# Kernel tuning notes

Hardware: AMD Instinct MI355X
Metric: run time of the kernel (lower is better)

The kernel has to match this reference:

```python
import jax, jax.numpy as jnp
import numpy as np

B, S, D, DV = 1, 4096, 1024, 1024  # S == 4*D required by the data-dependent scale broadcast


def setup_inputs() -> dict:
    key = jax.random.key(0)
    kq, kk, kv, ks, kp = jax.random.split(key, 5)
    return {
        "q": jax.random.normal(kq, (B, S, D), dtype=jnp.float32),
        "k": jax.random.normal(kk, (B, S, D), dtype=jnp.float32),
        "v": jax.random.normal(kv, (B, S, DV), dtype=jnp.float32),
        "scale_factor": jax.random.normal(ks, (1,), dtype=jnp.float32),  # overwritten in forward
        "dropout_p": jax.random.uniform(kp, (1,), dtype=jnp.float32),   # overwritten in forward
    }


def reference(q, k, v, scale_factor, dropout_p):
    b, s, d = q.shape
    step = s // 4
    # data-dependent per-column scale: 4 strided rows of q flattened -> (B, 4*D) == (B, S)
    scale = q[:, ::step].reshape(b, -1)            # (B, S)
    qk = jnp.einsum('bsd,btd->bst', q, k)           # (B, S, S)
    scaled_qk = qk * scale[:, None, :]              # torch broadcast (B,S)->(1,1,S) since B==1
    softmax_qk = jax.nn.softmax(scaled_qk, axis=-1)
    # dropout with tensor p is ill-defined in torch; identity (eval semantics)
    return jnp.einsum('bst,btv->bsv', softmax_qk, v)
```

## Files before the change

kernel.cpp:

```cpp
#include <hip/hip_runtime.h>
#include <hip/hip_bf16.h>

typedef __bf16 bf16x8 __attribute__((ext_vector_type(8)));
typedef __bf16 bf16x4 __attribute__((ext_vector_type(4)));
typedef float f32x4 __attribute__((ext_vector_type(4)));

#define S_LEN 4096
#define DDIM  1024

#define MFMA __builtin_amdgcn_mfma_f32_16x16x32_bf16

#define BAR() do { asm volatile("" ::: "memory"); __builtin_amdgcn_s_barrier(); asm volatile("" ::: "memory"); } while (0)
#define VM6() asm volatile("s_waitcnt vmcnt(6)" ::: "memory")
#define VM0() asm volatile("s_waitcnt vmcnt(0)" ::: "memory")

__device__ __forceinline__ void gl_lds16(const __bf16* g, __bf16* l)
{
    __builtin_amdgcn_global_load_lds(
        (const __attribute__((address_space(1))) void*)g,
        (__attribute__((address_space(3))) void*)l, 16, 0, 0);
}

__global__ void prep_hilo(const float* __restrict__ q, const float* __restrict__ kk,
                          __bf16* __restrict__ qh, __bf16* __restrict__ ql,
                          __bf16* __restrict__ kh, __bf16* __restrict__ kl)
{
    const int n8 = (S_LEN * DDIM) / 8;
    for (int i = blockIdx.x * blockDim.x + threadIdx.x; i < n8; i += gridDim.x * blockDim.x) {
        float4 a = *(const float4*)(q + (size_t)i * 8);
        float4 b = *(const float4*)(q + (size_t)i * 8 + 4);
        float va[8] = {a.x, a.y, a.z, a.w, b.x, b.y, b.z, b.w};
        bf16x8 h, l;
#pragma unroll
        for (int j = 0; j < 8; ++j) {
            __bf16 hh = (__bf16)va[j];
            h[j] = hh;
            l[j] = (__bf16)(va[j] - (float)hh);
        }
        *(bf16x8*)(qh + (size_t)i * 8) = h;
        *(bf16x8*)(ql + (size_t)i * 8) = l;

        a = *(const float4*)(kk + (size_t)i * 8);
        b = *(const float4*)(kk + (size_t)i * 8 + 4);
        float vb[8] = {a.x, a.y, a.z, a.w, b.x, b.y, b.z, b.w};
#pragma unroll
        for (int j = 0; j < 8; ++j) {
            __bf16 hh = (__bf16)vb[j];
            h[j] = hh;
            l[j] = (__bf16)(vb[j] - (float)hh);
        }
        *(bf16x8*)(kh + (size_t)i * 8) = h;
        *(bf16x8*)(kl + (size_t)i * 8) = l;
    }
}

__global__ void prep_vt(const float* __restrict__ v, __bf16* __restrict__ vt)
{
    __shared__ float tile[32][33];
    const int t0 = blockIdx.x * 32;
    const int d0 = blockIdx.y * 32;
    const int tx = threadIdx.x & 31;
    const int ty = threadIdx.x >> 5;
#pragma unroll
    for (int i = 0; i < 32; i += 8)
        tile[ty + i][tx] = v[(size_t)(t0 + ty + i) * DDIM + d0 + tx];
    __syncthreads();
#pragma unroll
    for (int i = 0; i < 32; i += 8)
        vt[(size_t)(d0 + ty + i) * S_LEN + t0 + tx] = (__bf16)tile[tx][ty + i];
}

__global__ void prep_scale(const float* __restrict__ q, float* __restrict__ scale)
{
    const int j = blockIdx.x * blockDim.x + threadIdx.x;
    if (j < S_LEN) scale[j] = q[((size_t)(j >> 10) << 20) + (j & 1023)];
}

__device__ __forceinline__ const __bf16* selA(const __bf16* qh, const __bf16* ql, int ps)
{ return ps == 1 ? ql : qh; }
__device__ __forceinline__ const __bf16* selB(const __bf16* kh, const __bf16* kl, int ps)
{ return ps == 2 ? kl : kh; }

template<int BUF, int RG>
__device__ __forceinline__ void stageG1(__bf16 (&lds)[2][4][8192], const __bf16* pl,
                                        int base, int koff, int w, int lane)
{
#pragma unroll
    for (int j = 0; j < 2; ++j) {
        const int ubase = (2 * w + j) * 64;
        const int u = ubase + lane;
        const int r = u >> 3, cu = u & 7;
        int grow;
        if (RG < 2) grow = base + ((r >> 6) << 7) + ((RG & 1) << 6) + (r & 63);
        else        grow = base + ((r >> 5) << 6) + ((RG & 1) << 5) + (r & 31);
        const __bf16* src = pl + (size_t)grow * DDIM + koff + ((cu ^ (r & 7)) << 3);
        gl_lds16(src, &lds[BUF][RG][0] + ubase * 8);
    }
}

template<int BUF, int MH>
__device__ __forceinline__ void rdA(bf16x8 (&a)[4][2], const __bf16 (&lds)[2][4][8192],
                                    int wr, int arow, int aoct)
{
#pragma unroll
    for (int mi = 0; mi < 4; ++mi)
#pragma unroll
        for (int ks = 0; ks < 2; ++ks) {
            const int lr = wr * 64 + mi * 16 + arow;
            const int cc = ks * 4 + aoct;
            a[mi][ks] = *(const bf16x8*)((const char*)&lds[BUF][MH][0]
                            + lr * 128 + ((cc ^ (lr & 7)) << 4));
        }
}

template<int BUF, int NH>
__device__ __forceinline__ void rdB(bf16x8 (&b)[2][2], const __bf16 (&lds)[2][4][8192],
                                    int wc, int arow, int aoct)
{
#pragma unroll
    for (int ni = 0; ni < 2; ++ni)
#pragma unroll
        for (int ks = 0; ks < 2; ++ks) {
            const int lr = wc * 32 + ni * 16 + arow;
            const int cc = ks * 4 + aoct;
            b[ni][ks] = *(const bf16x8*)((const char*)&lds[BUF][2 + NH][0]
                            + lr * 128 + ((cc ^ (lr & 7)) << 4));
        }
}

#define QMFMA(MH, NH, bb) \
    _Pragma("unroll") for (int ks = 0; ks < 2; ++ks) \
    _Pragma("unroll") for (int mi = 0; mi < 4; ++mi) \
    _Pragma("unroll") for (int ni = 0; ni < 2; ++ni) \
        acc[(MH)*4 + mi][(NH)*2 + ni] = MFMA(a[mi][ks], bb[ni][ks], acc[(MH)*4 + mi][(NH)*2 + ni], 0, 0, 0);

__global__ __launch_bounds__(512, 2) void gemm_qk(
    const __bf16* __restrict__ qh, const __bf16* __restrict__ ql,
    const __bf16* __restrict__ kh, const __bf16* __restrict__ kl,
    const float* __restrict__ scale, float* __restrict__ Sout)
{
    __shared__ __align__(16) __bf16 lds[2][4][8192];

    const int tid = threadIdx.x;
    const int w = tid >> 6, lane = tid & 63;
    const int arow = lane & 15, aoct = lane >> 4;
    const int wr = w >> 2, wc = w & 3;
    const int nb = (blockIdx.x & 7) * 32 + (blockIdx.x >> 3);
    const int m0 = (nb & 15) * 256, n0 = (nb >> 4) * 256;

    f32x4 acc[8][4];
#pragma unroll
    for (int i = 0; i < 8; ++i)
#pragma unroll
        for (int j = 0; j < 4; ++j) acc[i][j] = (f32x4){0.f, 0.f, 0.f, 0.f};

    stageG1<0, 0>(lds, selA(qh, ql, 0), m0, 0, w, lane);
    stageG1<0, 1>(lds, selA(qh, ql, 0), m0, 0, w, lane);
    stageG1<0, 2>(lds, selB(kh, kl, 0), n0, 0, w, lane);
    stageG1<0, 3>(lds, selB(kh, kl, 0), n0, 0, w, lane);
    stageG1<1, 0>(lds, selA(qh, ql, 0), m0, 64, w, lane);
    stageG1<1, 2>(lds, selB(kh, kl, 0), n0, 64, w, lane);
    stageG1<1, 3>(lds, selB(kh, kl, 0), n0, 64, w, lane);
    VM6(); BAR();

    for (int it = 0; it < 24; ++it) {
        const int t0 = 2 * it, t1 = 2 * it + 1;
        const bool last = (it == 23);
        const int ps1 = t1 >> 4, ko1 = (t1 & 15) << 6;
        const int ps2 = (t0 + 2) >> 4, ko2 = ((t0 + 2) & 15) << 6;
        const int ps3 = (t1 + 2) >> 4, ko3 = ((t1 + 2) & 15) << 6;
        bf16x8 a[4][2], b0[2][2], b1[2][2];

        rdA<0, 0>(a, lds, wr, arow, aoct);
        rdB<0, 0>(b0, lds, wc, arow, aoct);
        stageG1<1, 1>(lds, selA(qh, ql, ps1), m0, ko1, w, lane);
        BAR();
        __builtin_amdgcn_s_setprio(1); QMFMA(0, 0, b0); __builtin_amdgcn_s_setprio(0);
        BAR();
        rdB<0, 1>(b1, lds, wc, arow, aoct);
        if (!last) stageG1<0, 0>(lds, selA(qh, ql, ps2), m0, ko2, w, lane);
        BAR();
        __builtin_amdgcn_s_setprio(1); QMFMA(0, 1, b1); __builtin_amdgcn_s_setprio(0);
        BAR();
        rdA<0, 1>(a, lds, wr, arow, aoct);
        if (!last) stageG1<0, 2>(lds, selB(kh, kl, ps2), n0, ko2, w, lane);
        BAR();
        __builtin_amdgcn_s_setprio(1); QMFMA(1, 0, b0); __builtin_amdgcn_s_setprio(0);
        BAR();
        if (!last) stageG1<0, 3>(lds, selB(kh, kl, ps2), n0, ko2, w, lane);
        if (last) { VM0(); } else { VM6(); }
        BAR();
        __builtin_amdgcn_s_setprio(1); QMFMA(1, 1, b1); __builtin_amdgcn_s_setprio(0);
        BAR();
        rdA<1, 0>(a, lds, wr, arow, aoct);
        rdB<1, 0>(b0, lds, wc, arow, aoct);
        if (!last) stageG1<0, 1>(lds, selA(qh, ql, ps2), m0, ko2, w, lane);
        BAR();
        __builtin_amdgcn_s_setprio(1); QMFMA(0, 0, b0); __builtin_amdgcn_s_setprio(0);
        BAR();
        rdB<1, 1>(b1, lds, wc, arow, aoct);
        if (!last) stageG1<1, 0>(lds, selA(qh, ql, ps3), m0, ko3, w, lane);
        BAR();
        __builtin_amdgcn_s_setprio(1); QMFMA(0, 1, b1); __builtin_amdgcn_s_setprio(0);
        BAR();
        rdA<1, 1>(a, lds, wr, arow, aoct);
        if (!last) stageG1<1, 2>(lds, selB(kh, kl, ps3), n0, ko3, w, lane);
        BAR();
        __builtin_amdgcn_s_setprio(1); QMFMA(1, 0, b0); __builtin_amdgcn_s_setprio(0);
        BAR();
        if (!last) stageG1<1, 3>(lds, selB(kh, kl, ps3), n0, ko3, w, lane);
        if (last) { VM0(); } else { VM6(); }
        BAR();
        __builtin_amdgcn_s_setprio(1); QMFMA(1, 1, b1); __builtin_amdgcn_s_setprio(0);
        BAR();
    }

    const int nbase = n0 + wc * 64;
    float sc[4];
#pragma unroll
    for (int ni = 0; ni < 4; ++ni) sc[ni] = scale[nbase + ni * 16 + arow];
#pragma unroll
    for (int mi = 0; mi < 8; ++mi)
#pragma unroll
        for (int ni = 0; ni < 4; ++ni)
#pragma unroll
            for (int ii = 0; ii < 4; ++ii) {
                const int m = m0 + wr * 128 + mi * 16 + aoct * 4 + ii;
                Sout[(size_t)m * S_LEN + nbase + ni * 16 + arow] = acc[mi][ni][ii] * sc[ni];
            }
}

__global__ __launch_bounds__(256) void softmax_kernel(const float* __restrict__ S,
                                                      __bf16* __restrict__ P)
{
    __shared__ float red[8];
    const int row = blockIdx.x, tid = threadIdx.x;
    const int w = tid >> 6, lane = tid & 63;
    const float* sr = S + (size_t)row * S_LEN;
    float4 v[4];
#pragma unroll
    for (int c = 0; c < 4; ++c) v[c] = *(const float4*)(sr + c * 1024 + tid * 4);
    float mx = -3e38f;
#pragma unroll
    for (int c = 0; c < 4; ++c)
        mx = fmaxf(mx, fmaxf(fmaxf(v[c].x, v[c].y), fmaxf(v[c].z, v[c].w)));
#pragma unroll
    for (int sh = 32; sh >= 1; sh >>= 1) mx = fmaxf(mx, __shfl_xor(mx, sh));
    if (lane == 0) red[w] = mx;
    __syncthreads();
    mx = fmaxf(fmaxf(red[0], red[1]), fmaxf(red[2], red[3]));

    float e[4][4];
    float sum = 0.f;
#pragma unroll
    for (int c = 0; c < 4; ++c) {
        e[c][0] = __expf(v[c].x - mx); e[c][1] = __expf(v[c].y - mx);
        e[c][2] = __expf(v[c].z - mx); e[c][3] = __expf(v[c].w - mx);
        sum += (e[c][0] + e[c][1]) + (e[c][2] + e[c][3]);
    }
#pragma unroll
    for (int sh = 32; sh >= 1; sh >>= 1) sum += __shfl_xor(sum, sh);
    if (lane == 0) red[4 + w] = sum;
    __syncthreads();
    sum = (red[4] + red[5]) + (red[6] + red[7]);
    const float inv = 1.f / sum;
#pragma unroll
    for (int c = 0; c < 4; ++c) {
        bf16x4 o = {(__bf16)(e[c][0] * inv), (__bf16)(e[c][1] * inv),
                    (__bf16)(e[c][2] * inv), (__bf16)(e[c][3] * inv)};
        *(bf16x4*)(P + (size_t)row * 8192 + c * 1024 + tid * 4) = o;
    }
}

template<int BUF>
__device__ __forceinline__ void stageG2(__bf16 (&lds)[2][2][8192],
                                        const __bf16* __restrict__ P,
                                        const __bf16* __restrict__ vt,
                                        int m0, int n0, int t, int w, int lane)
{
#pragma unroll
    for (int j = 0; j < 4; ++j) {
        const int ubase = (4 * w + j) * 64;
        const int u = ubase + lane;
        const int r = u >> 3, cu = u & 7;
        const int kc = t * 64 + ((cu ^ (r & 7)) << 3);
        gl_lds16(P + (size_t)(m0 + r) * 8192 + kc, &lds[BUF][0][0] + ubase * 8);
        gl_lds16(vt + (size_t)(n0 + r) * S_LEN + kc, &lds[BUF][1][0] + ubase * 8);
    }
}

__global__ __launch_bounds__(256, 2) void gemm_pv(const __bf16* __restrict__ P,
                                                  const __bf16* __restrict__ vt,
                                                  float* __restrict__ out)
{
    __shared__ __align__(16) __bf16 lds[2][2][8192];

    const int tid = threadIdx.x;
    const int w = tid >> 6, lane = tid & 63;
    const int arow = lane & 15, aoct = lane >> 4;
    const int wr = w >> 1, wc = w & 1;
    const int nb = (blockIdx.x & 7) * 32 + (blockIdx.x >> 3);
    const int m0 = (nb & 31) * 128, n0 = (nb >> 5) * 128;

    f32x4 acc[4][4];
#pragma unroll
    for (int i = 0; i < 4; ++i)
#pragma unroll
        for (int j = 0; j < 4; ++j) acc[i][j] = (f32x4){0.f, 0.f, 0.f, 0.f};

    stageG2<0>(lds, P, vt, m0, n0, 0, w, lane);
    VM0(); BAR();

    for (int t = 0; t < 64; ++t) {
        const int cur = t & 1;
        if (t < 63) {
            if (cur) stageG2<0>(lds, P, vt, m0, n0, t + 1, w, lane);
            else     stageG2<1>(lds, P, vt, m0, n0, t + 1, w, lane);
        }
        bf16x8 a[4][2], b[4][2];
#pragma unroll
        for (int mi = 0; mi < 4; ++mi)
#pragma unroll
            for (int ks = 0; ks < 2; ++ks) {
                const int lr = wr * 64 + mi * 16 + arow;
                const int cc = ks * 4 + aoct;
                a[mi][ks] = *(const bf16x8*)((const char*)&lds[cur][0][0]
                                + lr * 128 + ((cc ^ (lr & 7)) << 4));
            }
#pragma unroll
        for (int ni = 0; ni < 4; ++ni)
#pragma unroll
            for (int ks = 0; ks < 2; ++ks) {
                const int lr = wc * 64 + ni * 16 + arow;
                const int cc = ks * 4 + aoct;
                b[ni][ks] = *(const bf16x8*)((const char*)&lds[cur][1][0]
                                + lr * 128 + ((cc ^ (lr & 7)) << 4));
            }
        __builtin_amdgcn_s_setprio(1);
#pragma unroll
        for (int ks = 0; ks < 2; ++ks)
#pragma unroll
            for (int mi = 0; mi < 4; ++mi)
#pragma unroll
                for (int ni = 0; ni < 4; ++ni)
                    acc[mi][ni] = MFMA(a[mi][ks], b[ni][ks], acc[mi][ni], 0, 0, 0);
        __builtin_amdgcn_s_setprio(0);
        VM0(); BAR();
    }

#pragma unroll
    for (int mi = 0; mi < 4; ++mi)
#pragma unroll
        for (int ni = 0; ni < 4; ++ni)
#pragma unroll
            for (int ii = 0; ii < 4; ++ii) {
                const int m = m0 + wr * 64 + mi * 16 + aoct * 4 + ii;
                const int n = n0 + wc * 64 + ni * 16 + arow;
                out[(size_t)m * DDIM + n] = acc[mi][ni][ii];
            }
}

extern "C" void kernel_launch(void* const* d_in, const int* in_sizes, int n_in,
                              void* d_out, int out_size, void* d_ws, size_t ws_size,
                              hipStream_t stream)
{
    const float* q = (const float*)d_in[0];
    const float* k = (const float*)d_in[1];
    const float* v = (const float*)d_in[2];
    float* out = (float*)d_out;

    const size_t PLANE = (size_t)S_LEN * DDIM * sizeof(__bf16);
    const size_t SOFF  = 5 * PLANE + 64 * 1024;
    const size_t NEEDED = SOFF + (size_t)S_LEN * S_LEN * sizeof(float);
    if (ws_size < NEEDED) return;

    char* ws = (char*)d_ws;
    __bf16* qh = (__bf16*)(ws);
    __bf16* ql = (__bf16*)(ws + PLANE);
    __bf16* kh = (__bf16*)(ws + 2 * PLANE);
    __bf16* kl = (__bf16*)(ws + 3 * PLANE);
    __bf16* vt = (__bf16*)(ws + 4 * PLANE);
    float* scale = (float*)(ws + 5 * PLANE);
    float* Smat = (float*)(ws + SOFF);
    __bf16* P = (__bf16*)Smat;

    prep_hilo<<<dim3(1024), dim3(256), 0, stream>>>(q, k, qh, ql, kh, kl);
    prep_vt<<<dim3(S_LEN / 32, DDIM / 32), dim3(256), 0, stream>>>(v, vt);
    prep_scale<<<dim3(4), dim3(1024), 0, stream>>>(q, scale);
    gemm_qk<<<dim3(256), dim3(512), 0, stream>>>(qh, ql, kh, kl, scale, Smat);
    softmax_kernel<<<dim3(S_LEN), dim3(256), 0, stream>>>(Smat, P);
    gemm_pv<<<dim3(256), dim3(256), 0, stream>>>(P, vt, out);
}
```

Measured before the change: 173.5 us.

## Triple-buffer PV GEMM with 8 waves and fold scale prep into hilo kernel

Restructures the P·V GEMM to 512 threads (8 waves, 2x4 wave grid, each wave owning 64x32) with a three-stage LDS ring. Loads run two K-steps ahead and use a partial vmcnt wait, so global-to-LDS transfers overlap MFMA work instead of draining every iteration. Separately, the scale gather is folded into prep_hilo, which removes one kernel launch. The trade-off is more LDS per block (96KB), a limit of one block per CU, and more barriers per iteration.

```diff
diff --git a/kernel.cpp b/kernel.cpp
--- a/kernel.cpp
+++ b/kernel.cpp
@@ -12,6 +12,7 @@
 
 #define BAR() do { asm volatile("" ::: "memory"); __builtin_amdgcn_s_barrier(); asm volatile("" ::: "memory"); } while (0)
 #define VM6() asm volatile("s_waitcnt vmcnt(6)" ::: "memory")
+#define VM4() asm volatile("s_waitcnt vmcnt(4)" ::: "memory")
 #define VM0() asm volatile("s_waitcnt vmcnt(0)" ::: "memory")
 
 __device__ __forceinline__ void gl_lds16(const __bf16* g, __bf16* l)
@@ -23,10 +24,14 @@
 
 __global__ void prep_hilo(const float* __restrict__ q, const float* __restrict__ kk,
                           __bf16* __restrict__ qh, __bf16* __restrict__ ql,
-                          __bf16* __restrict__ kh, __bf16* __restrict__ kl)
-{
+                          __bf16* __restrict__ kh, __bf16* __restrict__ kl,
+                          float* __restrict__ scale)
+{
+    const int gid = blockIdx.x * blockDim.x + threadIdx.x;
+    if (gid < S_LEN) scale[gid] = q[((size_t)(gid >> 10) << 20) + (gid & 1023)];
+
     const int n8 = (S_LEN * DDIM) / 8;
-    for (int i = blockIdx.x * blockDim.x + threadIdx.x; i < n8; i += gridDim.x * blockDim.x) {
+    for (int i = gid; i < n8; i += gridDim.x * blockDim.x) {
         float4 a = *(const float4*)(q + (size_t)i * 8);
         float4 b = *(const float4*)(q + (size_t)i * 8 + 4);
         float va[8] = {a.x, a.y, a.z, a.w, b.x, b.y, b.z, b.w};
@@ -68,12 +73,6 @@
 #pragma unroll
     for (int i = 0; i < 32; i += 8)
         vt[(size_t)(d0 + ty + i) * S_LEN + t0 + tx] = (__bf16)tile[tx][ty + i];
-}
-
-__global__ void prep_scale(const float* __restrict__ q, float* __restrict__ scale)
-{
-    const int j = blockIdx.x * blockDim.x + threadIdx.x;
-    if (j < S_LEN) scale[j] = q[((size_t)(j >> 10) << 20) + (j & 1023)];
 }
 
 __device__ __forceinline__ const __bf16* selA(const __bf16* qh, const __bf16* ql, int ps)
@@ -272,90 +271,91 @@
     }
 }
 
-template<int BUF>
-__device__ __forceinline__ void stageG2(__bf16 (&lds)[2][2][8192],
+__device__ __forceinline__ void stagePV(__bf16* __restrict__ dst,
                                         const __bf16* __restrict__ P,
                                         const __bf16* __restrict__ vt,
                                         int m0, int n0, int t, int w, int lane)
 {
 #pragma unroll
-    for (int j = 0; j < 4; ++j) {
-        const int ubase = (4 * w + j) * 64;
+    for (int j = 0; j < 2; ++j) {
+        const int ubase = (2 * w + j) * 64;
         const int u = ubase + lane;
         const int r = u >> 3, cu = u & 7;
         const int kc = t * 64 + ((cu ^ (r & 7)) << 3);
-        gl_lds16(P + (size_t)(m0 + r) * 8192 + kc, &lds[BUF][0][0] + ubase * 8);
-        gl_lds16(vt + (size_t)(n0 + r) * S_LEN + kc, &lds[BUF][1][0] + ubase * 8);
-    }
-}
-
-__global__ __launch_bounds__(256, 2) void gemm_pv(const __bf16* __restrict__ P,
+        gl_lds16(P + (size_t)(m0 + r) * 8192 + kc, dst + ubase * 8);
+        gl_lds16(vt + (size_t)(n0 + r) * S_LEN + kc, dst + 8192 + ubase * 8);
+    }
+}
+
+__global__ __launch_bounds__(512, 1) void gemm_pv(const __bf16* __restrict__ P,
                                                   const __bf16* __restrict__ vt,
                                                   float* __restrict__ out)
 {
-    __shared__ __align__(16) __bf16 lds[2][2][8192];
+    __shared__ __align__(16) __bf16 lds[3][2][8192];
 
     const int tid = threadIdx.x;
     const int w = tid >> 6, lane = tid & 63;
     const int arow = lane & 15, aoct = lane >> 4;
-    const int wr = w >> 1, wc = w & 1;
+    const int wr = w >> 2, wc = w & 3;
     const int nb = (blockIdx.x & 7) * 32 + (blockIdx.x >> 3);
     const int m0 = (nb & 31) * 128, n0 = (nb >> 5) * 128;
 
-    f32x4 acc[4][4];
+    f32x4 acc[4][2];
 #pragma unroll
     for (int i = 0; i < 4; ++i)
 #pragma unroll
-        for (int j = 0; j < 4; ++j) acc[i][j] = (f32x4){0.f, 0.f, 0.f, 0.f};
-
-    stageG2<0>(lds, P, vt, m0, n0, 0, w, lane);
-    VM0(); BAR();
-
+        for (int j = 0; j < 2; ++j) acc[i][j] = (f32x4){0.f, 0.f, 0.f, 0.f};
+
+    stagePV(&lds[0][0][0], P, vt, m0, n0, 0, w, lane);
+    stagePV(&lds[1][0][0], P, vt, m0, n0, 1, w, lane);
+    VM4(); BAR();
+
+    int c0 = 0, c1 = 1, c2 = 2;
     for (int t = 0; t < 64; ++t) {
-        const int cur = t & 1;
-        if (t < 63) {
-            if (cur) stageG2<0>(lds, P, vt, m0, n0, t + 1, w, lane);
-            else     stageG2<1>(lds, P, vt, m0, n0, t + 1, w, lane);
-        }
-        bf16x8 a[4][2], b[4][2];
+        const char* pa = (const char*)&lds[c0][0][0];
+        const char* pb = (const char*)&lds[c0][1][0];
+        bf16x8 a[4][2], b[2][2];
 #pragma unroll
         for (int mi = 0; mi < 4; ++mi)
 #pragma unroll
             for (int ks = 0; ks < 2; ++ks) {
                 const int lr = wr * 64 + mi * 16 + arow;
                 const int cc = ks * 4 + aoct;
-                a[mi][ks] = *(const bf16x8*)((const char*)&lds[cur][0][0]
-                                + lr * 128 + ((cc ^ (lr & 7)) << 4));
+                a[mi][ks] = *(const bf16x8*)(pa + lr * 128 + ((cc ^ (lr & 7)) << 4));
             }
 #pragma unroll
-        for (int ni = 0; ni < 4; ++ni)
+        for (int ni = 0; ni < 2; ++ni)
 #pragma unroll
             for (int ks = 0; ks < 2; ++ks) {
-                const int lr = wc * 64 + ni * 16 + arow;
+                const int lr = wc * 32 + ni * 16 + arow;
                 const int cc = ks * 4 + aoct;
-                b[ni][ks] = *(const bf16x8*)((const char*)&lds[cur][1][0]
-                                + lr * 128 + ((cc ^ (lr & 7)) << 4));
+                b[ni][ks] = *(const bf16x8*)(pb + lr * 128 + ((cc ^ (lr & 7)) << 4));
             }
+        if (t < 62) stagePV(&lds[c2][0][0], P, vt, m0, n0, t + 2, w, lane);
+        BAR();
         __builtin_amdgcn_s_setprio(1);
 #pragma unroll
         for (int ks = 0; ks < 2; ++ks)
 #pragma unroll
             for (int mi = 0; mi < 4; ++mi)
 #pragma unroll
-                for (int ni = 0; ni < 4; ++ni)
+                for (int ni = 0; ni < 2; ++ni)
                     acc[mi][ni] = MFMA(a[mi][ks], b[ni][ks], acc[mi][ni], 0, 0, 0);
         __builtin_amdgcn_s_setprio(0);
-        VM0(); BAR();
+        __builtin_amdgcn_sched_barrier(0);
+        if (t <= 60) { VM4(); } else { VM0(); }
+        BAR();
+        const int tmp = c0; c0 = c1; c1 = c2; c2 = tmp;
     }
 
 #pragma unroll
     for (int mi = 0; mi < 4; ++mi)
 #pragma unroll
-        for (int ni = 0; ni < 4; ++ni)
+        for (int ni = 0; ni < 2; ++ni)
 #pragma unroll
             for (int ii = 0; ii < 4; ++ii) {
                 const int m = m0 + wr * 64 + mi * 16 + aoct * 4 + ii;
-                const int n = n0 + wc * 64 + ni * 16 + arow;
+                const int n = n0 + wc * 32 + ni * 16 + arow;
                 out[(size_t)m * DDIM + n] = acc[mi][ni][ii];
             }
 }
@@ -384,10 +384,9 @@
     float* Smat = (float*)(ws + SOFF);
     __bf16* P = (__bf16*)Smat;
 
-    prep_hilo<<<dim3(1024), dim3(256), 0, stream>>>(q, k, qh, ql, kh, kl);
+    prep_hilo<<<dim3(1024), dim3(256), 0, stream>>>(q, k, qh, ql, kh, kl, scale);
     prep_vt<<<dim3(S_LEN / 32, DDIM / 32), dim3(256), 0, stream>>>(v, vt);
-    prep_scale<<<dim3(4), dim3(1024), 0, stream>>>(q, scale);
     gemm_qk<<<dim3(256), dim3(512), 0, stream>>>(qh, ql, kh, kl, scale, Smat);
     softmax_kernel<<<dim3(S_LEN), dim3(256), 0, stream>>>(Smat, P);
-    gemm_pv<<<dim3(256), dim3(256), 0, stream>>>(P, vt, out);
-}
+    gemm_pv<<<dim3(256), dim3(512), 0, stream>>>(P, vt, out);
+}
```

After: 164.6 us. -5.1%, faster.
